# Optimization experiments

Hardware: AMD Instinct MI355X
Metric: run time of the kernel (lower is better)

Reference implementation:

```python
import jax, jax.numpy as jnp
import numpy as np
import math

H, DK, DV = 16, 64, 64
D = H * DK  # model_dimension = 1024
N = M = L = 2048


def setup_inputs() -> dict:
    key = jax.random.key(0)
    ks = jax.random.split(key, 12)
    s = 1.0 / math.sqrt(DK)  # keep softmax logits in a sane range
    return {
        "queries": jax.random.normal(ks[0], (N, DK), jnp.float32),
        "keys": jax.random.normal(ks[1], (M, DK), jnp.float32),
        "values": jax.random.normal(ks[2], (L, DV), jnp.float32),
        "Wq": jax.random.normal(ks[3], (H, DK, D), jnp.float32) * s,
        "bq": jax.random.normal(ks[4], (H, D), jnp.float32) * 0.02,
        "Wk": jax.random.normal(ks[5], (H, DK, D), jnp.float32) * s,
        "bk": jax.random.normal(ks[6], (H, D), jnp.float32) * 0.02,
        "Wv": jax.random.normal(ks[7], (H, DV, D), jnp.float32) * s,
        "bv": jax.random.normal(ks[8], (H, D), jnp.float32) * 0.02,
        "Wo": jax.random.normal(ks[9], (D, H * DV), jnp.float32) * (1.0 / math.sqrt(H * DV)),
        "bo": jax.random.normal(ks[10], (D,), jnp.float32) * 0.02,
    }


def reference(queries, keys, values, Wq, bq, Wk, bk, Wv, bv, Wo, bo):
    # Batched per-head projections (original loops over heads in Python).
    Qp = jnp.einsum("nk,hkd->hnd", queries, Wq) + bq[:, None, :]   # (H, N, D)
    Kp = jnp.einsum("mk,hkd->hmd", keys, Wk) + bk[:, None, :]      # (H, M, D)
    Vp = jnp.einsum("lv,hvd->hld", values, Wv) + bv[:, None, :]    # (H, M, D)
    scores = jnp.einsum("hnd,hmd->hnm", Qp, Kp) / math.sqrt(DK)
    attn = jax.nn.softmax(scores, axis=-1)
    heads_out = jnp.einsum("hnm,hmd->hnd", attn, Vp)               # (H, N, D)
    # torch.concat(heads, dim=0).sum(dim=0) == sum over heads AND rows -> (D,)
    pooled = heads_out.sum(axis=(0, 1)).reshape(1, D)
    return pooled @ Wo.T + bo  # (1, D)
```

## Files before the change

kernel.cpp:

```cpp
#include <hip/hip_runtime.h>


typedef __attribute__((ext_vector_type(4))) float floatx4;
typedef __attribute__((ext_vector_type(8))) short shortx8;

__device__ inline unsigned short f2bf(float f) {
    unsigned int u = __float_as_uint(f);
    u += 0x7FFFu + ((u >> 16) & 1u);
    return (unsigned short)(u >> 16);
}
__device__ inline float bf2f(unsigned short s) {
    return __uint_as_float(((unsigned int)s) << 16);
}

#define SWZ(row, bc) ((row) * 128 + ((bc) ^ (((row) & 7) << 4)))
#define QSCALE 0.18033688f

__global__ __launch_bounds__(256) void prep_kernel(
    const float* __restrict__ Wq, const float* __restrict__ Wk,
    const float* __restrict__ bq, const float* __restrict__ keys,
    float* __restrict__ Apart, float* __restrict__ vhpart,
    unsigned short* __restrict__ Kb, float* __restrict__ r_ws) {
    const int tid = threadIdx.x;
    const int bx = blockIdx.x;
    __shared__ __align__(16) unsigned char sm[36352];
    if (bx < 128) {
        const int g = bx >> 4, h = bx & 15;
        const int c0 = g * 128;
        unsigned short* wq = (unsigned short*)sm;
        unsigned short* wk = (unsigned short*)(sm + 17408);
        float* bqs = (float*)(sm + 34816);
        float* vred = (float*)(sm + 35328);
        {
            int row = tid >> 2, cs = (tid & 3) * 32;
            const float* wqp = Wq + (size_t)(h * 64 + row) * 1024 + c0 + cs;
            const float* wkp = Wk + (size_t)(h * 64 + row) * 1024 + c0 + cs;
            #pragma unroll
            for (int u = 0; u < 8; ++u) {
                float4 a = *(const float4*)&wqp[u * 4];
                float4 b = *(const float4*)&wkp[u * 4];
                *(ushort4*)&wq[row * 136 + cs + u * 4] =
                    (ushort4){f2bf(a.x), f2bf(a.y), f2bf(a.z), f2bf(a.w)};
                *(ushort4*)&wk[row * 136 + cs + u * 4] =
                    (ushort4){f2bf(b.x), f2bf(b.y), f2bf(b.z), f2bf(b.w)};
            }
            if (tid < 128) bqs[tid] = bq[h * 1024 + c0 + tid];
        }
        __syncthreads();
        const int w = tid >> 6, lane = tid & 63;
        const int ln = lane & 15, quad = lane >> 4;
        {
            const int j = tid & 63, half = tid >> 6;
            float accv = 0.f;
            #pragma unroll
            for (int u = 0; u < 32; ++u)
                accv += bf2f(wk[j * 136 + half * 32 + u]) * bqs[half * 32 + u];
            vred[half * 64 + j] = accv;
        }
        shortx8 af[4];
        #pragma unroll
        for (int kk = 0; kk < 4; ++kk)
            af[kk] = *(shortx8*)&wq[(w * 16 + ln) * 136 + kk * 32 + quad * 8];
        float* ap = Apart + (size_t)bx * 4096;
        #pragma unroll
        for (int cn = 0; cn < 4; ++cn) {
            floatx4 acc = {};
            #pragma unroll
            for (int kk = 0; kk < 4; ++kk) {
                shortx8 bf_ = *(shortx8*)&wk[(cn * 16 + ln) * 136 + kk * 32 + quad * 8];
                acc = __builtin_amdgcn_mfma_f32_16x16x32_bf16(af[kk], bf_, acc, 0, 0, 0);
            }
            #pragma unroll
            for (int r = 0; r < 4; ++r)
                ap[(w * 16 + quad * 4 + r) * 64 + cn * 16 + ln] = acc[r];
        }
        __syncthreads();
        if (tid < 64)
            vhpart[bx * 64 + tid] = vred[tid] + vred[64 + tid] +
                                    vred[128 + tid] + vred[192 + tid];
    } else {
        int bk = bx - 128;
        int base = (bk * 256 + tid) * 32;
        #pragma unroll
        for (int u = 0; u < 8; ++u) {
            float4 a = *(const float4*)&keys[base + u * 4];
            *(ushort4*)&Kb[base + u * 4] =
                (ushort4){f2bf(a.x), f2bf(a.y), f2bf(a.z), f2bf(a.w)};
        }
        if (tid < 64) r_ws[bk * 64 + tid] = 0.f;
    }
}

__global__ __launch_bounds__(256) void reduceA_kernel(
    const float* __restrict__ Apart, const float* __restrict__ vhpart,
    unsigned short* __restrict__ Atlg, float* __restrict__ vhg) {
    const int tid = threadIdx.x;
    const int h = blockIdx.x >> 2, uq = blockIdx.x & 3;
    #pragma unroll
    for (int uu = 0; uu < 4; ++uu) {
        int e = (uq * 4 + uu) * 256 + tid;
        float s = 0.f;
        #pragma unroll
        for (int g = 0; g < 8; ++g)
            s += Apart[g * 65536 + h * 4096 + e];
        Atlg[h * 4096 + (e & 63) * 64 + (e >> 6)] = f2bf(s);
    }
    if (uq == 0 && tid < 64) {
        float s = 0.f;
        #pragma unroll
        for (int g = 0; g < 8; ++g) s += vhpart[(g * 16 + h) * 64 + tid];
        vhg[h * 64 + tid] = s;
    }
}

__global__ __launch_bounds__(256, 4) void pass1_kernel(
    const float* __restrict__ queries, const unsigned short* __restrict__ Atlg,
    const float* __restrict__ vhg, const unsigned short* __restrict__ Kb,
    unsigned short* __restrict__ Qhs, float* __restrict__ u_ws) {
    const int h = blockIdx.y;
    const int n0 = blockIdx.x * 64;
    const int tid = threadIdx.x;
    const int w = tid >> 6, lane = tid & 63;
    const int ln = lane & 15, quad = lane >> 4;

    __shared__ __align__(16) unsigned char lds[33792];
    __shared__ float vhs[64];
    unsigned short* qstage = (unsigned short*)lds;
    unsigned short* Atl = (unsigned short*)(lds + 9216);
    unsigned short* qh = (unsigned short*)(lds + 24576);

    {
        int row = tid >> 2, c16 = (tid & 3) * 16;
        const float* qp = queries + (size_t)(n0 + row) * 64 + c16;
        #pragma unroll
        for (int u = 0; u < 4; ++u) {
            float4 a = *(const float4*)&qp[u * 4];
            *(ushort4*)&qstage[row * 72 + c16 + u * 4] =
                (ushort4){f2bf(a.x), f2bf(a.y), f2bf(a.z), f2bf(a.w)};
        }
        #pragma unroll
        for (int u = 0; u < 2; ++u)
            *(shortx8*)&Atl[row * 72 + c16 + u * 8] =
                *(const shortx8*)&Atlg[h * 4096 + row * 64 + c16 + u * 8];
    }
    if (tid < 64) vhs[tid] = vhg[h * 64 + tid];
    __syncthreads();

    {
        shortx8 qa[2];
        #pragma unroll
        for (int kk = 0; kk < 2; ++kk)
            qa[kk] = *(shortx8*)&qstage[(w * 16 + ln) * 72 + kk * 32 + quad * 8];
        #pragma unroll
        for (int cn = 0; cn < 4; ++cn) {
            floatx4 acc = {};
            #pragma unroll
            for (int kk = 0; kk < 2; ++kk) {
                shortx8 bfr = *(shortx8*)&Atl[(cn * 16 + ln) * 72 + kk * 32 + quad * 8];
                acc = __builtin_amdgcn_mfma_f32_16x16x32_bf16(qa[kk], bfr, acc, 0, 0, 0);
            }
            #pragma unroll
            for (int r = 0; r < 4; ++r)
                qh[(w * 16 + quad * 4 + r) * 72 + cn * 16 + ln] =
                    f2bf((acc[r] + vhs[cn * 16 + ln]) * QSCALE);
        }
    }
    __syncthreads();

    #pragma unroll
    for (int k = 0; k < 2; ++k) {
        int seg = tid * 2 + k, row = seg >> 3, off = (seg & 7) * 8;
        *(shortx8*)&Qhs[((size_t)h * 2048 + n0 + row) * 64 + off] =
            *(shortx8*)&qh[row * 72 + off];
    }
    const int srow = tid >> 2, sc = (tid & 3) * 16;
    #pragma unroll
    for (int i = 0; i < 2; ++i)
        *(shortx8*)(lds + SWZ(srow, sc * 2 + i * 16)) =
            *(const shortx8*)&Kb[(size_t)srow * 64 + sc + i * 8];
    shortx8 kr[2];
    #pragma unroll
    for (int i = 0; i < 2; ++i)
        kr[i] = *(const shortx8*)&Kb[(size_t)(64 + srow) * 64 + sc + i * 8];
    shortx8 qf[2];
    #pragma unroll
    for (int kk = 0; kk < 2; ++kk)
        qf[kk] = *(shortx8*)&qh[(w * 16 + ln) * 72 + kk * 32 + quad * 8];
    __syncthreads();

    float lacc[4] = {};
    int rb = 0;
    for (int s = 0; s < 32; ++s) {
        const unsigned char* kb = lds + rb * 8192;
        const int wb = (rb == 2) ? 0 : rb + 1;
        if (s < 31) {
            #pragma unroll
            for (int i = 0; i < 2; ++i)
                *(shortx8*)(lds + wb * 8192 + SWZ(srow, sc * 2 + i * 16)) = kr[i];
        }
        if (s < 30) {
            int m0n = (s + 2) * 64;
            #pragma unroll
            for (int i = 0; i < 2; ++i)
                kr[i] = *(const shortx8*)&Kb[(size_t)(m0n + srow) * 64 + sc + i * 8];
        }
        #pragma unroll
        for (int cm = 0; cm < 4; ++cm) {
            shortx8 kf0 = *(const shortx8*)(kb + SWZ(cm * 16 + ln, quad * 16));
            shortx8 kf1 = *(const shortx8*)(kb + SWZ(cm * 16 + ln, 64 + quad * 16));
            floatx4 acc = {};
            acc = __builtin_amdgcn_mfma_f32_16x16x32_bf16(qf[0], kf0, acc, 0, 0, 0);
            acc = __builtin_amdgcn_mfma_f32_16x16x32_bf16(qf[1], kf1, acc, 0, 0, 0);
            #pragma unroll
            for (int r = 0; r < 4; ++r)
                lacc[r] += __builtin_amdgcn_exp2f(acc[r]);
        }
        __syncthreads();
        rb = wb;
    }

    #pragma unroll
    for (int r = 0; r < 4; ++r) {
        float x = lacc[r];
        #pragma unroll
        for (int o = 1; o <= 8; o <<= 1) x += __shfl_xor(x, o);
        if (ln == 0)
            u_ws[(size_t)h * 2048 + n0 + w * 16 + quad * 4 + r] = 1.0f / x;
    }
}

__global__ __launch_bounds__(256, 4) void pass2_kernel(
    const unsigned short* __restrict__ Qhs, const float* __restrict__ u_ws,
    const unsigned short* __restrict__ Kb, const float* __restrict__ values,
    float* __restrict__ r_ws) {
    const int h = blockIdx.y;
    const int mb = blockIdx.x * 64;
    const int tid = threadIdx.x;
    const int w = tid >> 6, lane = tid & 63;
    const int ln = lane & 15, quad = lane >> 4;

    __shared__ __align__(16) unsigned char lds[26624];
    float* u_sb = (float*)(lds + 24576);
    float* g_s = (float*)(lds + 25344);
    float* Rred = (float*)(lds + 25600);

    shortx8 kf[2];
    #pragma unroll
    for (int kk = 0; kk < 2; ++kk)
        kf[kk] = *(const shortx8*)&Kb[(size_t)(mb + w * 16 + ln) * 64 + kk * 32 + quad * 8];

    const int srow = tid >> 2, sc = (tid & 3) * 16;
    #pragma unroll
    for (int i = 0; i < 2; ++i)
        *(shortx8*)(lds + SWZ(srow, sc * 2 + i * 16)) =
            *(const shortx8*)&Qhs[((size_t)h * 2048 + srow) * 64 + sc + i * 8];
    if (tid < 64) u_sb[tid] = u_ws[(size_t)h * 2048 + tid];
    shortx8 qrn[2];
    float urn = 0.f;
    #pragma unroll
    for (int i = 0; i < 2; ++i)
        qrn[i] = *(const shortx8*)&Qhs[((size_t)h * 2048 + 64 + srow) * 64 + sc + i * 8];
    if (tid < 64) urn = u_ws[(size_t)h * 2048 + 64 + tid];
    __syncthreads();

    float gacc = 0.f;
    int rb = 0;
    for (int s = 0; s < 32; ++s) {
        const unsigned char* qb = lds + rb * 8192;
        const float* us = u_sb + rb * 64;
        const int wb = (rb == 2) ? 0 : rb + 1;
        if (s < 31) {
            #pragma unroll
            for (int i = 0; i < 2; ++i)
                *(shortx8*)(lds + wb * 8192 + SWZ(srow, sc * 2 + i * 16)) = qrn[i];
            if (tid < 64) u_sb[wb * 64 + tid] = urn;
        }
        if (s < 30) {
            int n0n = (s + 2) * 64;
            #pragma unroll
            for (int i = 0; i < 2; ++i)
                qrn[i] = *(const shortx8*)&Qhs[((size_t)h * 2048 + n0n + srow) * 64 + sc + i * 8];
            if (tid < 64) urn = u_ws[(size_t)h * 2048 + n0n + tid];
        }
        #pragma unroll
        for (int rt = 0; rt < 4; ++rt) {
            shortx8 qa0 = *(const shortx8*)(qb + SWZ(rt * 16 + ln, quad * 16));
            shortx8 qa1 = *(const shortx8*)(qb + SWZ(rt * 16 + ln, 64 + quad * 16));
            floatx4 acc = {};
            acc = __builtin_amdgcn_mfma_f32_16x16x32_bf16(qa0, kf[0], acc, 0, 0, 0);
            acc = __builtin_amdgcn_mfma_f32_16x16x32_bf16(qa1, kf[1], acc, 0, 0, 0);
            #pragma unroll
            for (int r = 0; r < 4; ++r)
                gacc += __builtin_amdgcn_exp2f(acc[r]) * us[rt * 16 + quad * 4 + r];
        }
        __syncthreads();
        rb = wb;
    }

    gacc += __shfl_xor(gacc, 16);
    gacc += __shfl_xor(gacc, 32);
    if (quad == 0) g_s[w * 16 + ln] = gacc;
    __syncthreads();
    {
        int grp = tid >> 6, v = tid & 63;
        float acc = 0.f;
        #pragma unroll
        for (int j = 0; j < 16; ++j)
            acc += g_s[grp * 16 + j] *
                   values[(size_t)(mb + grp * 16 + j) * 64 + v];
        Rred[grp * 64 + v] = acc;
    }
    __syncthreads();
    if (tid < 64)
        atomicAdd(&r_ws[h * 64 + tid],
                  Rred[tid] + Rred[64 + tid] + Rred[128 + tid] + Rred[192 + tid]);
}

__global__ __launch_bounds__(256) void pool_kernel(
    const float* __restrict__ Wv, const float* __restrict__ bv,
    const float* __restrict__ r_ws, float* __restrict__ pooled) {
    const int tid = threadIdx.x;
    const int d0 = blockIdx.x * 16;
    const int d = tid & 15, hh = tid >> 4;
    __shared__ float red[16][17];
    float acc = bv[hh * 1024 + d0 + d] * 2048.0f;
    const float* rv = r_ws + hh * 64;
    const float* wp = Wv + (size_t)hh * 64 * 1024 + d0 + d;
    #pragma unroll 8
    for (int v = 0; v < 64; ++v) acc += rv[v] * wp[(size_t)v * 1024];
    red[hh][d] = acc;
    __syncthreads();
    if (tid < 16) {
        float s = 0.f;
        #pragma unroll
        for (int g = 0; g < 16; ++g) s += red[g][tid];
        pooled[d0 + tid] = s;
    }
}

__global__ __launch_bounds__(256) void out_kernel(
    const float* __restrict__ Wo, const float* __restrict__ bo,
    const float* __restrict__ pooled, float* __restrict__ out) {
    const int tid = threadIdx.x, w = tid >> 6, lane = tid & 63;
    const int dp = blockIdx.x * 4 + w;
    const float* wr = Wo + (size_t)dp * 1024 + lane * 16;
    const float* pp = pooled + lane * 16;
    float acc = 0.f;
    #pragma unroll
    for (int u = 0; u < 4; ++u) {
        float4 a = *(const float4*)&wr[u * 4];
        float4 p = *(const float4*)&pp[u * 4];
        acc += a.x * p.x + a.y * p.y + a.z * p.z + a.w * p.w;
    }
    #pragma unroll
    for (int o = 32; o > 0; o >>= 1) acc += __shfl_xor(acc, o);
    if (lane == 0) out[dp] = acc + bo[dp];
}

extern "C" void kernel_launch(void* const* d_in, const int* in_sizes, int n_in,
                              void* d_out, int out_size, void* d_ws, size_t ws_size,
                              hipStream_t stream) {
    const float* queries = (const float*)d_in[0];
    const float* keys    = (const float*)d_in[1];
    const float* values  = (const float*)d_in[2];
    const float* Wq      = (const float*)d_in[3];
    const float* bq      = (const float*)d_in[4];
    const float* Wk      = (const float*)d_in[5];
    const float* Wv      = (const float*)d_in[7];
    const float* bv      = (const float*)d_in[8];
    const float* Wo      = (const float*)d_in[9];
    const float* bo      = (const float*)d_in[10];
    float* out = (float*)d_out;

    char* base = (char*)d_ws;
    unsigned short* Qhs = (unsigned short*)base;
    float* Apart  = (float*)base;
    float* vhpart = Apart + 524288;
    float* u_ws   = (float*)(base + 4194304);
    float* r_ws   = (float*)(base + 4325376);
    float* pooled = (float*)(base + 4329472);
    unsigned short* Kb   = (unsigned short*)(base + 4333568);
    unsigned short* Atlg = (unsigned short*)(base + 4595712);
    float* vhg    = (float*)(base + 4726784);

    prep_kernel<<<144, 256, 0, stream>>>(Wq, Wk, bq, keys,
                                         Apart, vhpart, Kb, r_ws);
    reduceA_kernel<<<64, 256, 0, stream>>>(Apart, vhpart, Atlg, vhg);
    pass1_kernel<<<dim3(32, 16), 256, 0, stream>>>(queries, Atlg, vhg,
                                                   Kb, Qhs, u_ws);
    pass2_kernel<<<dim3(32, 16), 256, 0, stream>>>(Qhs, u_ws, Kb, values, r_ws);
    pool_kernel<<<64, 256, 0, stream>>>(Wv, bv, r_ws, pooled);
    out_kernel<<<256, 256, 0, stream>>>(Wo, bo, pooled, out);
}
```

Measured before the change: 134.1 us.

## Fuse all six stages into one cooperative kernel with grid-wide syncs

Merges the prep, reduce, pass1, pass2, pool and output kernels into a single kernel launched cooperatively with 512 blocks. Stages are separated by grid.sync(), and each stage picks its work from the block index. This removes five kernel launches and the idle gaps between dependent launches. The cost is five grid-wide barriers, a single larger LDS allocation and a launch bound of two blocks per CU, which all 512 blocks must fit to stay co-resident.

New measurement: 432.1 us. 222% more time.

```diff
diff --git a/kernel.cpp b/kernel.cpp
--- a/kernel.cpp
+++ b/kernel.cpp
@@ -1,4 +1,7 @@
 #include <hip/hip_runtime.h>
+#include <hip/hip_cooperative_groups.h>
+
+namespace cg = cooperative_groups;
 
 
 typedef __attribute__((ext_vector_type(4))) float floatx4;
@@ -16,14 +19,22 @@
 #define SWZ(row, bc) ((row) * 128 + ((bc) ^ (((row) & 7) << 4)))
 #define QSCALE 0.18033688f
 
-__global__ __launch_bounds__(256) void prep_kernel(
+__global__ __launch_bounds__(256, 2) void fused_kernel(
     const float* __restrict__ Wq, const float* __restrict__ Wk,
     const float* __restrict__ bq, const float* __restrict__ keys,
+    const float* __restrict__ values, const float* __restrict__ queries,
+    const float* __restrict__ Wv, const float* __restrict__ bv,
+    const float* __restrict__ Wo, const float* __restrict__ bo,
     float* __restrict__ Apart, float* __restrict__ vhpart,
-    unsigned short* __restrict__ Kb, float* __restrict__ r_ws) {
+    unsigned short* __restrict__ Kb, unsigned short* __restrict__ Atlg,
+    float* __restrict__ vhg, unsigned short* __restrict__ Qhs,
+    float* __restrict__ u_ws, float* __restrict__ r_ws,
+    float* __restrict__ pooled, float* __restrict__ out) {
+    cg::grid_group grid = cg::this_grid();
     const int tid = threadIdx.x;
     const int bx = blockIdx.x;
-    __shared__ __align__(16) unsigned char sm[36352];
+    __shared__ __align__(16) unsigned char sm[36608];
+
     if (bx < 128) {
         const int g = bx >> 4, h = bx & 15;
         const int c0 = g * 128;
@@ -78,7 +89,7 @@
         if (tid < 64)
             vhpart[bx * 64 + tid] = vred[tid] + vred[64 + tid] +
                                     vred[128 + tid] + vred[192 + tid];
-    } else {
+    } else if (bx < 144) {
         int bk = bx - 128;
         int base = (bk * 256 + tid) * 32;
         #pragma unroll
@@ -89,272 +100,256 @@
         }
         if (tid < 64) r_ws[bk * 64 + tid] = 0.f;
     }
-}
-
-__global__ __launch_bounds__(256) void reduceA_kernel(
-    const float* __restrict__ Apart, const float* __restrict__ vhpart,
-    unsigned short* __restrict__ Atlg, float* __restrict__ vhg) {
-    const int tid = threadIdx.x;
-    const int h = blockIdx.x >> 2, uq = blockIdx.x & 3;
-    #pragma unroll
-    for (int uu = 0; uu < 4; ++uu) {
-        int e = (uq * 4 + uu) * 256 + tid;
-        float s = 0.f;
-        #pragma unroll
-        for (int g = 0; g < 8; ++g)
-            s += Apart[g * 65536 + h * 4096 + e];
-        Atlg[h * 4096 + (e & 63) * 64 + (e >> 6)] = f2bf(s);
-    }
-    if (uq == 0 && tid < 64) {
-        float s = 0.f;
-        #pragma unroll
-        for (int g = 0; g < 8; ++g) s += vhpart[(g * 16 + h) * 64 + tid];
-        vhg[h * 64 + tid] = s;
-    }
-}
-
-__global__ __launch_bounds__(256, 4) void pass1_kernel(
-    const float* __restrict__ queries, const unsigned short* __restrict__ Atlg,
-    const float* __restrict__ vhg, const unsigned short* __restrict__ Kb,
-    unsigned short* __restrict__ Qhs, float* __restrict__ u_ws) {
-    const int h = blockIdx.y;
-    const int n0 = blockIdx.x * 64;
-    const int tid = threadIdx.x;
-    const int w = tid >> 6, lane = tid & 63;
-    const int ln = lane & 15, quad = lane >> 4;
-
-    __shared__ __align__(16) unsigned char lds[33792];
-    __shared__ float vhs[64];
-    unsigned short* qstage = (unsigned short*)lds;
-    unsigned short* Atl = (unsigned short*)(lds + 9216);
-    unsigned short* qh = (unsigned short*)(lds + 24576);
+    grid.sync();
+
+    if (bx < 64) {
+        const int h = bx >> 2, uq = bx & 3;
+        #pragma unroll
+        for (int uu = 0; uu < 4; ++uu) {
+            int e = (uq * 4 + uu) * 256 + tid;
+            float s = 0.f;
+            #pragma unroll
+            for (int g = 0; g < 8; ++g)
+                s += Apart[g * 65536 + h * 4096 + e];
+            Atlg[h * 4096 + (e & 63) * 64 + (e >> 6)] = f2bf(s);
+        }
+        if (uq == 0 && tid < 64) {
+            float s = 0.f;
+            #pragma unroll
+            for (int g = 0; g < 8; ++g) s += vhpart[(g * 16 + h) * 64 + tid];
+            vhg[h * 64 + tid] = s;
+        }
+    }
+    grid.sync();
 
     {
-        int row = tid >> 2, c16 = (tid & 3) * 16;
-        const float* qp = queries + (size_t)(n0 + row) * 64 + c16;
+        const int h = bx >> 5;
+        const int n0 = (bx & 31) * 64;
+        const int w = tid >> 6, lane = tid & 63;
+        const int ln = lane & 15, quad = lane >> 4;
+        unsigned short* qstage = (unsigned short*)sm;
+        unsigned short* Atl = (unsigned short*)(sm + 9216);
+        unsigned short* qh = (unsigned short*)(sm + 24576);
+        float* vhs = (float*)(sm + 33792);
+
+        {
+            int row = tid >> 2, c16 = (tid & 3) * 16;
+            const float* qp = queries + (size_t)(n0 + row) * 64 + c16;
+            #pragma unroll
+            for (int u = 0; u < 4; ++u) {
+                float4 a = *(const float4*)&qp[u * 4];
+                *(ushort4*)&qstage[row * 72 + c16 + u * 4] =
+                    (ushort4){f2bf(a.x), f2bf(a.y), f2bf(a.z), f2bf(a.w)};
+            }
+            #pragma unroll
+            for (int u = 0; u < 2; ++u)
+                *(shortx8*)&Atl[row * 72 + c16 + u * 8] =
+                    *(const shortx8*)&Atlg[h * 4096 + row * 64 + c16 + u * 8];
+        }
+        if (tid < 64) vhs[tid] = vhg[h * 64 + tid];
+        __syncthreads();
+
+        {
+            shortx8 qa[2];
+            #pragma unroll
+            for (int kk = 0; kk < 2; ++kk)
+                qa[kk] = *(shortx8*)&qstage[(w * 16 + ln) * 72 + kk * 32 + quad * 8];
+            #pragma unroll
+            for (int cn = 0; cn < 4; ++cn) {
+                floatx4 acc = {};
+                #pragma unroll
+                for (int kk = 0; kk < 2; ++kk) {
+                    shortx8 bfr = *(shortx8*)&Atl[(cn * 16 + ln) * 72 + kk * 32 + quad * 8];
+                    acc = __builtin_amdgcn_mfma_f32_16x16x32_bf16(qa[kk], bfr, acc, 0, 0, 0);
+                }
+                #pragma unroll
+                for (int r = 0; r < 4; ++r)
+                    qh[(w * 16 + quad * 4 + r) * 72 + cn * 16 + ln] =
+                        f2bf((acc[r] + vhs[cn * 16 + ln]) * QSCALE);
+            }
+        }
+        __syncthreads();
+
+        #pragma unroll
+        for (int k = 0; k < 2; ++k) {
+            int seg = tid * 2 + k, row = seg >> 3, off = (seg & 7) * 8;
+            *(shortx8*)&Qhs[((size_t)h * 2048 + n0 + row) * 64 + off] =
+                *(shortx8*)&qh[row * 72 + off];
+        }
+        const int srow = tid >> 2, sc = (tid & 3) * 16;
+        #pragma unroll
+        for (int i = 0; i < 2; ++i)
+            *(shortx8*)(sm + SWZ(srow, sc * 2 + i * 16)) =
+                *(const shortx8*)&Kb[(size_t)srow * 64 + sc + i * 8];
+        shortx8 kr[2];
+        #pragma unroll
+        for (int i = 0; i < 2; ++i)
+            kr[i] = *(const shortx8*)&Kb[(size_t)(64 + srow) * 64 + sc + i * 8];
+        shortx8 qf[2];
+        #pragma unroll
+        for (int kk = 0; kk < 2; ++kk)
+            qf[kk] = *(shortx8*)&qh[(w * 16 + ln) * 72 + kk * 32 + quad * 8];
+        __syncthreads();
+
+        float lacc[4] = {};
+        int rb = 0;
+        for (int s = 0; s < 32; ++s) {
+            const unsigned char* kb = sm + rb * 8192;
+            const int wb = (rb == 2) ? 0 : rb + 1;
+            if (s < 31) {
+                #pragma unroll
+                for (int i = 0; i < 2; ++i)
+                    *(shortx8*)(sm + wb * 8192 + SWZ(srow, sc * 2 + i * 16)) = kr[i];
+            }
+            if (s < 30) {
+                int m0n = (s + 2) * 64;
+                #pragma unroll
+                for (int i = 0; i < 2; ++i)
+                    kr[i] = *(const shortx8*)&Kb[(size_t)(m0n + srow) * 64 + sc + i * 8];
+            }
+            #pragma unroll
+            for (int cm = 0; cm < 4; ++cm) {
+                shortx8 kf0 = *(const shortx8*)(kb + SWZ(cm * 16 + ln, quad * 16));
+                shortx8 kf1 = *(const shortx8*)(kb + SWZ(cm * 16 + ln, 64 + quad * 16));
+                floatx4 acc = {};
+                acc = __builtin_amdgcn_mfma_f32_16x16x32_bf16(qf[0], kf0, acc, 0, 0, 0);
+                acc = __builtin_amdgcn_mfma_f32_16x16x32_bf16(qf[1], kf1, acc, 0, 0, 0);
+                #pragma unroll
+                for (int r = 0; r < 4; ++r)
+                    lacc[r] += __builtin_amdgcn_exp2f(acc[r]);
+            }
+            __syncthreads();
+            rb = wb;
+        }
+        #pragma unroll
+        for (int r = 0; r < 4; ++r) {
+            float x = lacc[r];
+            #pragma unroll
+            for (int o = 1; o <= 8; o <<= 1) x += __shfl_xor(x, o);
+            if (ln == 0)
+                u_ws[(size_t)h * 2048 + n0 + w * 16 + quad * 4 + r] = 1.0f / x;
+        }
+    }
+    grid.sync();
+
+    {
+        const int h = bx >> 5;
+        const int mb = (bx & 31) * 64;
+        const int w = tid >> 6, lane = tid & 63;
+        const int ln = lane & 15, quad = lane >> 4;
+        float* u_sb = (float*)(sm + 24576);
+        float* g_s = (float*)(sm + 25344);
+        float* Rred = (float*)(sm + 25600);
+
+        shortx8 kf[2];
+        #pragma unroll
+        for (int kk = 0; kk < 2; ++kk)
+            kf[kk] = *(const shortx8*)&Kb[(size_t)(mb + w * 16 + ln) * 64 + kk * 32 + quad * 8];
+
+        const int srow = tid >> 2, sc = (tid & 3) * 16;
+        #pragma unroll
+        for (int i = 0; i < 2; ++i)
+            *(shortx8*)(sm + SWZ(srow, sc * 2 + i * 16)) =
+                *(const shortx8*)&Qhs[((size_t)h * 2048 + srow) * 64 + sc + i * 8];
+        if (tid < 64) u_sb[tid] = u_ws[(size_t)h * 2048 + tid];
+        shortx8 qrn[2];
+        float urn = 0.f;
+        #pragma unroll
+        for (int i = 0; i < 2; ++i)
+            qrn[i] = *(const shortx8*)&Qhs[((size_t)h * 2048 + 64 + srow) * 64 + sc + i * 8];
+        if (tid < 64) urn = u_ws[(size_t)h * 2048 + 64 + tid];
+        __syncthreads();
+
+        float gacc = 0.f;
+        int rb = 0;
+        for (int s = 0; s < 32; ++s) {
+            const unsigned char* qb = sm + rb * 8192;
+            const float* us = u_sb + rb * 64;
+            const int wb = (rb == 2) ? 0 : rb + 1;
+            if (s < 31) {
+                #pragma unroll
+                for (int i = 0; i < 2; ++i)
+                    *(shortx8*)(sm + wb * 8192 + SWZ(srow, sc * 2 + i * 16)) = qrn[i];
+                if (tid < 64) u_sb[wb * 64 + tid] = urn;
+            }
+            if (s < 30) {
+                int n0n = (s + 2) * 64;
+                #pragma unroll
+                for (int i = 0; i < 2; ++i)
+                    qrn[i] = *(const shortx8*)&Qhs[((size_t)h * 2048 + n0n + srow) * 64 + sc + i * 8];
+                if (tid < 64) urn = u_ws[(size_t)h * 2048 + n0n + tid];
+            }
+            #pragma unroll
+            for (int rt = 0; rt < 4; ++rt) {
+                shortx8 qa0 = *(const shortx8*)(qb + SWZ(rt * 16 + ln, quad * 16));
+                shortx8 qa1 = *(const shortx8*)(qb + SWZ(rt * 16 + ln, 64 + quad * 16));
+                floatx4 acc = {};
+                acc = __builtin_amdgcn_mfma_f32_16x16x32_bf16(qa0, kf[0], acc, 0, 0, 0);
+                acc = __builtin_amdgcn_mfma_f32_16x16x32_bf16(qa1, kf[1], acc, 0, 0, 0);
+                #pragma unroll
+                for (int r = 0; r < 4; ++r)
+                    gacc += __builtin_amdgcn_exp2f(acc[r]) * us[rt * 16 + quad * 4 + r];
+            }
+            __syncthreads();
+            rb = wb;
+        }
+
+        gacc += __shfl_xor(gacc, 16);
+        gacc += __shfl_xor(gacc, 32);
+        if (quad == 0) g_s[w * 16 + ln] = gacc;
+        __syncthreads();
+        {
+            int grp = tid >> 6, v = tid & 63;
+            float acc = 0.f;
+            #pragma unroll
+            for (int j = 0; j < 16; ++j)
+                acc += g_s[grp * 16 + j] *
+                       values[(size_t)(mb + grp * 16 + j) * 64 + v];
+            Rred[grp * 64 + v] = acc;
+        }
+        __syncthreads();
+        if (tid < 64)
+            atomicAdd(&r_ws[h * 64 + tid],
+                      Rred[tid] + Rred[64 + tid] + Rred[128 + tid] + Rred[192 + tid]);
+    }
+    grid.sync();
+
+    if (bx < 64) {
+        const int d0 = bx * 16;
+        const int d = tid & 15, hh = tid >> 4;
+        float* red = (float*)sm;
+        float acc = bv[hh * 1024 + d0 + d] * 2048.0f;
+        const float* rv = r_ws + hh * 64;
+        const float* wp = Wv + (size_t)hh * 64 * 1024 + d0 + d;
+        #pragma unroll 8
+        for (int v = 0; v < 64; ++v) acc += rv[v] * wp[(size_t)v * 1024];
+        red[hh * 17 + d] = acc;
+        __syncthreads();
+        if (tid < 16) {
+            float s = 0.f;
+            #pragma unroll
+            for (int g = 0; g < 16; ++g) s += red[g * 17 + tid];
+            pooled[d0 + tid] = s;
+        }
+    }
+    grid.sync();
+
+    if (bx < 256) {
+        const int w = tid >> 6, lane = tid & 63;
+        const int dp = bx * 4 + w;
+        const float* wr = Wo + (size_t)dp * 1024 + lane * 16;
+        const float* pp = pooled + lane * 16;
+        float acc = 0.f;
         #pragma unroll
         for (int u = 0; u < 4; ++u) {
-            float4 a = *(const float4*)&qp[u * 4];
-            *(ushort4*)&qstage[row * 72 + c16 + u * 4] =
-                (ushort4){f2bf(a.x), f2bf(a.y), f2bf(a.z), f2bf(a.w)};
-        }
-        #pragma unroll
-        for (int u = 0; u < 2; ++u)
-            *(shortx8*)&Atl[row * 72 + c16 + u * 8] =
-                *(const shortx8*)&Atlg[h * 4096 + row * 64 + c16 + u * 8];
-    }
-    if (tid < 64) vhs[tid] = vhg[h * 64 + tid];
-    __syncthreads();
-
-    {
-        shortx8 qa[2];
-        #pragma unroll
-        for (int kk = 0; kk < 2; ++kk)
-            qa[kk] = *(shortx8*)&qstage[(w * 16 + ln) * 72 + kk * 32 + quad * 8];
-        #pragma unroll
-        for (int cn = 0; cn < 4; ++cn) {
-            floatx4 acc = {};
-            #pragma unroll
-            for (int kk = 0; kk < 2; ++kk) {
-                shortx8 bfr = *(shortx8*)&Atl[(cn * 16 + ln) * 72 + kk * 32 + quad * 8];
-                acc = __builtin_amdgcn_mfma_f32_16x16x32_bf16(qa[kk], bfr, acc, 0, 0, 0);
-            }
-            #pragma unroll
-            for (int r = 0; r < 4; ++r)
-                qh[(w * 16 + quad * 4 + r) * 72 + cn * 16 + ln] =
-                    f2bf((acc[r] + vhs[cn * 16 + ln]) * QSCALE);
-        }
-    }
-    __syncthreads();
-
-    #pragma unroll
-    for (int k = 0; k < 2; ++k) {
-        int seg = tid * 2 + k, row = seg >> 3, off = (seg & 7) * 8;
-        *(shortx8*)&Qhs[((size_t)h * 2048 + n0 + row) * 64 + off] =
-            *(shortx8*)&qh[row * 72 + off];
-    }
-    const int srow = tid >> 2, sc = (tid & 3) * 16;
-    #pragma unroll
-    for (int i = 0; i < 2; ++i)
-        *(shortx8*)(lds + SWZ(srow, sc * 2 + i * 16)) =
-            *(const shortx8*)&Kb[(size_t)srow * 64 + sc + i * 8];
-    shortx8 kr[2];
-    #pragma unroll
-    for (int i = 0; i < 2; ++i)
-        kr[i] = *(const shortx8*)&Kb[(size_t)(64 + srow) * 64 + sc + i * 8];
-    shortx8 qf[2];
-    #pragma unroll
-    for (int kk = 0; kk < 2; ++kk)
-        qf[kk] = *(shortx8*)&qh[(w * 16 + ln) * 72 + kk * 32 + quad * 8];
-    __syncthreads();
-
-    float lacc[4] = {};
-    int rb = 0;
-    for (int s = 0; s < 32; ++s) {
-        const unsigned char* kb = lds + rb * 8192;
-        const int wb = (rb == 2) ? 0 : rb + 1;
-        if (s < 31) {
-            #pragma unroll
-            for (int i = 0; i < 2; ++i)
-                *(shortx8*)(lds + wb * 8192 + SWZ(srow, sc * 2 + i * 16)) = kr[i];
-        }
-        if (s < 30) {
-            int m0n = (s + 2) * 64;
-            #pragma unroll
-            for (int i = 0; i < 2; ++i)
-                kr[i] = *(const shortx8*)&Kb[(size_t)(m0n + srow) * 64 + sc + i * 8];
-        }
-        #pragma unroll
-        for (int cm = 0; cm < 4; ++cm) {
-            shortx8 kf0 = *(const shortx8*)(kb + SWZ(cm * 16 + ln, quad * 16));
-            shortx8 kf1 = *(const shortx8*)(kb + SWZ(cm * 16 + ln, 64 + quad * 16));
-            floatx4 acc = {};
-            acc = __builtin_amdgcn_mfma_f32_16x16x32_bf16(qf[0], kf0, acc, 0, 0, 0);
-            acc = __builtin_amdgcn_mfma_f32_16x16x32_bf16(qf[1], kf1, acc, 0, 0, 0);
-            #pragma unroll
-            for (int r = 0; r < 4; ++r)
-                lacc[r] += __builtin_amdgcn_exp2f(acc[r]);
-        }
-        __syncthreads();
-        rb = wb;
-    }
-
-    #pragma unroll
-    for (int r = 0; r < 4; ++r) {
-        float x = lacc[r];
-        #pragma unroll
-        for (int o = 1; o <= 8; o <<= 1) x += __shfl_xor(x, o);
-        if (ln == 0)
-            u_ws[(size_t)h * 2048 + n0 + w * 16 + quad * 4 + r] = 1.0f / x;
-    }
-}
-
-__global__ __launch_bounds__(256, 4) void pass2_kernel(
-    const unsigned short* __restrict__ Qhs, const float* __restrict__ u_ws,
-    const unsigned short* __restrict__ Kb, const float* __restrict__ values,
-    float* __restrict__ r_ws) {
-    const int h = blockIdx.y;
-    const int mb = blockIdx.x * 64;
-    const int tid = threadIdx.x;
-    const int w = tid >> 6, lane = tid & 63;
-    const int ln = lane & 15, quad = lane >> 4;
-
-    __shared__ __align__(16) unsigned char lds[26624];
-    float* u_sb = (float*)(lds + 24576);
-    float* g_s = (float*)(lds + 25344);
-    float* Rred = (float*)(lds + 25600);
-
-    shortx8 kf[2];
-    #pragma unroll
-    for (int kk = 0; kk < 2; ++kk)
-        kf[kk] = *(const shortx8*)&Kb[(size_t)(mb + w * 16 + ln) * 64 + kk * 32 + quad * 8];
-
-    const int srow = tid >> 2, sc = (tid & 3) * 16;
-    #pragma unroll
-    for (int i = 0; i < 2; ++i)
-        *(shortx8*)(lds + SWZ(srow, sc * 2 + i * 16)) =
-            *(const shortx8*)&Qhs[((size_t)h * 2048 + srow) * 64 + sc + i * 8];
-    if (tid < 64) u_sb[tid] = u_ws[(size_t)h * 2048 + tid];
-    shortx8 qrn[2];
-    float urn = 0.f;
-    #pragma unroll
-    for (int i = 0; i < 2; ++i)
-        qrn[i] = *(const shortx8*)&Qhs[((size_t)h * 2048 + 64 + srow) * 64 + sc + i * 8];
-    if (tid < 64) urn = u_ws[(size_t)h * 2048 + 64 + tid];
-    __syncthreads();
-
-    float gacc = 0.f;
-    int rb = 0;
-    for (int s = 0; s < 32; ++s) {
-        const unsigned char* qb = lds + rb * 8192;
-        const float* us = u_sb + rb * 64;
-        const int wb = (rb == 2) ? 0 : rb + 1;
-        if (s < 31) {
-            #pragma unroll
-            for (int i = 0; i < 2; ++i)
-                *(shortx8*)(lds + wb * 8192 + SWZ(srow, sc * 2 + i * 16)) = qrn[i];
-            if (tid < 64) u_sb[wb * 64 + tid] = urn;
-        }
-        if (s < 30) {
-            int n0n = (s + 2) * 64;
-            #pragma unroll
-            for (int i = 0; i < 2; ++i)
-                qrn[i] = *(const shortx8*)&Qhs[((size_t)h * 2048 + n0n + srow) * 64 + sc + i * 8];
-            if (tid < 64) urn = u_ws[(size_t)h * 2048 + n0n + tid];
-        }
-        #pragma unroll
-        for (int rt = 0; rt < 4; ++rt) {
-            shortx8 qa0 = *(const shortx8*)(qb + SWZ(rt * 16 + ln, quad * 16));
-            shortx8 qa1 = *(const shortx8*)(qb + SWZ(rt * 16 + ln, 64 + quad * 16));
-            floatx4 acc = {};
-            acc = __builtin_amdgcn_mfma_f32_16x16x32_bf16(qa0, kf[0], acc, 0, 0, 0);
-            acc = __builtin_amdgcn_mfma_f32_16x16x32_bf16(qa1, kf[1], acc, 0, 0, 0);
-            #pragma unroll
-            for (int r = 0; r < 4; ++r)
-                gacc += __builtin_amdgcn_exp2f(acc[r]) * us[rt * 16 + quad * 4 + r];
-        }
-        __syncthreads();
-        rb = wb;
-    }
-
-    gacc += __shfl_xor(gacc, 16);
-    gacc += __shfl_xor(gacc, 32);
-    if (quad == 0) g_s[w * 16 + ln] = gacc;
-    __syncthreads();
-    {
-        int grp = tid >> 6, v = tid & 63;
-        float acc = 0.f;
-        #pragma unroll
-        for (int j = 0; j < 16; ++j)
-            acc += g_s[grp * 16 + j] *
-                   values[(size_t)(mb + grp * 16 + j) * 64 + v];
-        Rred[grp * 64 + v] = acc;
-    }
-    __syncthreads();
-    if (tid < 64)
-        atomicAdd(&r_ws[h * 64 + tid],
-                  Rred[tid] + Rred[64 + tid] + Rred[128 + tid] + Rred[192 + tid]);
-}
-
-__global__ __launch_bounds__(256) void pool_kernel(
-    const float* __restrict__ Wv, const float* __restrict__ bv,
-    const float* __restrict__ r_ws, float* __restrict__ pooled) {
-    const int tid = threadIdx.x;
-    const int d0 = blockIdx.x * 16;
-    const int d = tid & 15, hh = tid >> 4;
-    __shared__ float red[16][17];
-    float acc = bv[hh * 1024 + d0 + d] * 2048.0f;
-    const float* rv = r_ws + hh * 64;
-    const float* wp = Wv + (size_t)hh * 64 * 1024 + d0 + d;
-    #pragma unroll 8
-    for (int v = 0; v < 64; ++v) acc += rv[v] * wp[(size_t)v * 1024];
-    red[hh][d] = acc;
-    __syncthreads();
-    if (tid < 16) {
-        float s = 0.f;
-        #pragma unroll
-        for (int g = 0; g < 16; ++g) s += red[g][tid];
-        pooled[d0 + tid] = s;
-    }
-}
-
-__global__ __launch_bounds__(256) void out_kernel(
-    const float* __restrict__ Wo, const float* __restrict__ bo,
-    const float* __restrict__ pooled, float* __restrict__ out) {
-    const int tid = threadIdx.x, w = tid >> 6, lane = tid & 63;
-    const int dp = blockIdx.x * 4 + w;
-    const float* wr = Wo + (size_t)dp * 1024 + lane * 16;
-    const float* pp = pooled + lane * 16;
-    float acc = 0.f;
-    #pragma unroll
-    for (int u = 0; u < 4; ++u) {
-        float4 a = *(const float4*)&wr[u * 4];
-        float4 p = *(const float4*)&pp[u * 4];
-        acc += a.x * p.x + a.y * p.y + a.z * p.z + a.w * p.w;
-    }
-    #pragma unroll
-    for (int o = 32; o > 0; o >>= 1) acc += __shfl_xor(acc, o);
-    if (lane == 0) out[dp] = acc + bo[dp];
+            float4 a = *(const float4*)&wr[u * 4];
+            float4 p = *(const float4*)&pp[u * 4];
+            acc += a.x * p.x + a.y * p.y + a.z * p.z + a.w * p.w;
+        }
+        #pragma unroll
+        for (int o = 32; o > 0; o >>= 1) acc += __shfl_xor(acc, o);
+        if (lane == 0) out[dp] = acc + bo[dp];
+    }
 }
 
 extern "C" void kernel_launch(void* const* d_in, const int* in_sizes, int n_in,
@@ -383,12 +378,11 @@
     unsigned short* Atlg = (unsigned short*)(base + 4595712);
     float* vhg    = (float*)(base + 4726784);
 
-    prep_kernel<<<144, 256, 0, stream>>>(Wq, Wk, bq, keys,
-                                         Apart, vhpart, Kb, r_ws);
-    reduceA_kernel<<<64, 256, 0, stream>>>(Apart, vhpart, Atlg, vhg);
-    pass1_kernel<<<dim3(32, 16), 256, 0, stream>>>(queries, Atlg, vhg,
-                                                   Kb, Qhs, u_ws);
-    pass2_kernel<<<dim3(32, 16), 256, 0, stream>>>(Qhs, u_ws, Kb, values, r_ws);
-    pool_kernel<<<64, 256, 0, stream>>>(Wv, bv, r_ws, pooled);
-    out_kernel<<<256, 256, 0, stream>>>(Wo, bo, pooled, out);
+    void* args[] = {
+        (void*)&Wq, (void*)&Wk, (void*)&bq, (void*)&keys, (void*)&values,
+        (void*)&queries, (void*)&Wv, (void*)&bv, (void*)&Wo, (void*)&bo,
+        (void*)&Apart, (void*)&vhpart, (void*)&Kb, (void*)&Atlg, (void*)&vhg,
+        (void*)&Qhs, (void*)&u_ws, (void*)&r_ws, (void*)&pooled, (void*)&out};
+    hipLaunchCooperativeKernel((void*)fused_kernel, dim3(512), dim3(256),
+                               args, 0, stream);
 }
```

## Halve row tile per block in pass1/pass2 and split columns across wave pairs

Applied to the files above, without the earlier changes.

Each block in pass1 and pass2 now handles 32 query or key rows instead of 64, so the grid doubles to 64x16 blocks. Pairs of waves split the column tiles of the streamed operand, and their partial row sums are combined through LDS. This is meant to fill the 256 CUs of the MI355X better (1024 blocks instead of 512). In exchange, each block streams the full K or Q operand for half the useful work, doubling global and LDS traffic per result, and adds a reduction step.

New measurement: 171.9 us. 28.1% more time.

```diff
diff --git a/kernel.cpp b/kernel.cpp
--- a/kernel.cpp
+++ b/kernel.cpp
@@ -118,30 +118,34 @@
     const float* __restrict__ vhg, const unsigned short* __restrict__ Kb,
     unsigned short* __restrict__ Qhs, float* __restrict__ u_ws) {
     const int h = blockIdx.y;
-    const int n0 = blockIdx.x * 64;
+    const int n0 = blockIdx.x * 32;
     const int tid = threadIdx.x;
     const int w = tid >> 6, lane = tid & 63;
     const int ln = lane & 15, quad = lane >> 4;
-
-    __shared__ __align__(16) unsigned char lds[33792];
+    const int t = w & 1, kh2 = w >> 1;
+
+    __shared__ __align__(16) unsigned char lds[29440];
     __shared__ float vhs[64];
     unsigned short* qstage = (unsigned short*)lds;
-    unsigned short* Atl = (unsigned short*)(lds + 9216);
+    unsigned short* Atl = (unsigned short*)(lds + 4608);
     unsigned short* qh = (unsigned short*)(lds + 24576);
+    float* lsum = (float*)(lds + 29184);
 
     {
-        int row = tid >> 2, c16 = (tid & 3) * 16;
-        const float* qp = queries + (size_t)(n0 + row) * 64 + c16;
-        #pragma unroll
-        for (int u = 0; u < 4; ++u) {
-            float4 a = *(const float4*)&qp[u * 4];
-            *(ushort4*)&qstage[row * 72 + c16 + u * 4] =
-                (ushort4){f2bf(a.x), f2bf(a.y), f2bf(a.z), f2bf(a.w)};
-        }
-        #pragma unroll
-        for (int u = 0; u < 2; ++u)
-            *(shortx8*)&Atl[row * 72 + c16 + u * 8] =
-                *(const shortx8*)&Atlg[h * 4096 + row * 64 + c16 + u * 8];
+        int row = tid >> 3, c8 = (tid & 7) * 8;
+        const float* qp = queries + (size_t)(n0 + row) * 64 + c8;
+        float4 a = *(const float4*)qp;
+        float4 b = *(const float4*)(qp + 4);
+        *(ushort4*)&qstage[row * 72 + c8] =
+            (ushort4){f2bf(a.x), f2bf(a.y), f2bf(a.z), f2bf(a.w)};
+        *(ushort4*)&qstage[row * 72 + c8 + 4] =
+            (ushort4){f2bf(b.x), f2bf(b.y), f2bf(b.z), f2bf(b.w)};
+    }
+    #pragma unroll
+    for (int k = 0; k < 2; ++k) {
+        int seg = tid * 2 + k, row = seg >> 3, off = (seg & 7) * 8;
+        *(shortx8*)&Atl[row * 72 + off] =
+            *(const shortx8*)&Atlg[h * 4096 + row * 64 + off];
     }
     if (tid < 64) vhs[tid] = vhg[h * 64 + tid];
     __syncthreads();
@@ -150,9 +154,10 @@
         shortx8 qa[2];
         #pragma unroll
         for (int kk = 0; kk < 2; ++kk)
-            qa[kk] = *(shortx8*)&qstage[(w * 16 + ln) * 72 + kk * 32 + quad * 8];
-        #pragma unroll
-        for (int cn = 0; cn < 4; ++cn) {
+            qa[kk] = *(shortx8*)&qstage[(t * 16 + ln) * 72 + kk * 32 + quad * 8];
+        #pragma unroll
+        for (int i = 0; i < 2; ++i) {
+            int cn = kh2 * 2 + i;
             floatx4 acc = {};
             #pragma unroll
             for (int kk = 0; kk < 2; ++kk) {
@@ -161,15 +166,14 @@
             }
             #pragma unroll
             for (int r = 0; r < 4; ++r)
-                qh[(w * 16 + quad * 4 + r) * 72 + cn * 16 + ln] =
+                qh[(t * 16 + quad * 4 + r) * 72 + cn * 16 + ln] =
                     f2bf((acc[r] + vhs[cn * 16 + ln]) * QSCALE);
         }
     }
     __syncthreads();
 
-    #pragma unroll
-    for (int k = 0; k < 2; ++k) {
-        int seg = tid * 2 + k, row = seg >> 3, off = (seg & 7) * 8;
+    {
+        int row = tid >> 3, off = (tid & 7) * 8;
         *(shortx8*)&Qhs[((size_t)h * 2048 + n0 + row) * 64 + off] =
             *(shortx8*)&qh[row * 72 + off];
     }
@@ -185,7 +189,7 @@
     shortx8 qf[2];
     #pragma unroll
     for (int kk = 0; kk < 2; ++kk)
-        qf[kk] = *(shortx8*)&qh[(w * 16 + ln) * 72 + kk * 32 + quad * 8];
+        qf[kk] = *(shortx8*)&qh[(t * 16 + ln) * 72 + kk * 32 + quad * 8];
     __syncthreads();
 
     float lacc[4] = {};
@@ -205,7 +209,8 @@
                 kr[i] = *(const shortx8*)&Kb[(size_t)(m0n + srow) * 64 + sc + i * 8];
         }
         #pragma unroll
-        for (int cm = 0; cm < 4; ++cm) {
+        for (int i = 0; i < 2; ++i) {
+            int cm = kh2 * 2 + i;
             shortx8 kf0 = *(const shortx8*)(kb + SWZ(cm * 16 + ln, quad * 16));
             shortx8 kf1 = *(const shortx8*)(kb + SWZ(cm * 16 + ln, 64 + quad * 16));
             floatx4 acc = {};
@@ -224,9 +229,11 @@
         float x = lacc[r];
         #pragma unroll
         for (int o = 1; o <= 8; o <<= 1) x += __shfl_xor(x, o);
-        if (ln == 0)
-            u_ws[(size_t)h * 2048 + n0 + w * 16 + quad * 4 + r] = 1.0f / x;
-    }
+        if (ln == 0) lsum[kh2 * 32 + t * 16 + quad * 4 + r] = x;
+    }
+    __syncthreads();
+    if (tid < 32)
+        u_ws[(size_t)h * 2048 + n0 + tid] = 1.0f / (lsum[tid] + lsum[32 + tid]);
 }
 
 __global__ __launch_bounds__(256, 4) void pass2_kernel(
@@ -234,20 +241,21 @@
     const unsigned short* __restrict__ Kb, const float* __restrict__ values,
     float* __restrict__ r_ws) {
     const int h = blockIdx.y;
-    const int mb = blockIdx.x * 64;
+    const int mb = blockIdx.x * 32;
     const int tid = threadIdx.x;
     const int w = tid >> 6, lane = tid & 63;
     const int ln = lane & 15, quad = lane >> 4;
+    const int t = w & 1, rh = w >> 1;
 
     __shared__ __align__(16) unsigned char lds[26624];
     float* u_sb = (float*)(lds + 24576);
-    float* g_s = (float*)(lds + 25344);
+    float* g_part = (float*)(lds + 25344);
     float* Rred = (float*)(lds + 25600);
 
     shortx8 kf[2];
     #pragma unroll
     for (int kk = 0; kk < 2; ++kk)
-        kf[kk] = *(const shortx8*)&Kb[(size_t)(mb + w * 16 + ln) * 64 + kk * 32 + quad * 8];
+        kf[kk] = *(const shortx8*)&Kb[(size_t)(mb + t * 16 + ln) * 64 + kk * 32 + quad * 8];
 
     const int srow = tid >> 2, sc = (tid & 3) * 16;
     #pragma unroll
@@ -283,7 +291,8 @@
             if (tid < 64) urn = u_ws[(size_t)h * 2048 + n0n + tid];
         }
         #pragma unroll
-        for (int rt = 0; rt < 4; ++rt) {
+        for (int i = 0; i < 2; ++i) {
+            int rt = rh * 2 + i;
             shortx8 qa0 = *(const shortx8*)(qb + SWZ(rt * 16 + ln, quad * 16));
             shortx8 qa1 = *(const shortx8*)(qb + SWZ(rt * 16 + ln, 64 + quad * 16));
             floatx4 acc = {};
@@ -299,15 +308,16 @@
 
     gacc += __shfl_xor(gacc, 16);
     gacc += __shfl_xor(gacc, 32);
-    if (quad == 0) g_s[w * 16 + ln] = gacc;
+    if (quad == 0) g_part[rh * 32 + t * 16 + ln] = gacc;
     __syncthreads();
     {
         int grp = tid >> 6, v = tid & 63;
         float acc = 0.f;
         #pragma unroll
-        for (int j = 0; j < 16; ++j)
-            acc += g_s[grp * 16 + j] *
-                   values[(size_t)(mb + grp * 16 + j) * 64 + v];
+        for (int j = 0; j < 8; ++j) {
+            float gs = g_part[grp * 8 + j] + g_part[32 + grp * 8 + j];
+            acc += gs * values[(size_t)(mb + grp * 8 + j) * 64 + v];
+        }
         Rred[grp * 64 + v] = acc;
     }
     __syncthreads();
@@ -386,9 +396,9 @@
     prep_kernel<<<144, 256, 0, stream>>>(Wq, Wk, bq, keys,
                                          Apart, vhpart, Kb, r_ws);
     reduceA_kernel<<<64, 256, 0, stream>>>(Apart, vhpart, Atlg, vhg);
-    pass1_kernel<<<dim3(32, 16), 256, 0, stream>>>(queries, Atlg, vhg,
+    pass1_kernel<<<dim3(64, 16), 256, 0, stream>>>(queries, Atlg, vhg,
                                                    Kb, Qhs, u_ws);
-    pass2_kernel<<<dim3(32, 16), 256, 0, stream>>>(Qhs, u_ws, Kb, values, r_ws);
+    pass2_kernel<<<dim3(64, 16), 256, 0, stream>>>(Qhs, u_ws, Kb, values, r_ws);
     pool_kernel<<<64, 256, 0, stream>>>(Wv, bv, r_ws, pooled);
     out_kernel<<<256, 256, 0, stream>>>(Wo, bo, pooled, out);
 }
```
